# Kernel tuning notes

Measured on AMD Instinct MI355X. Metric: run time of the kernel, lower is better.

The kernel has to match this reference:

```python
import jax, jax.numpy as jnp
import numpy as np
import math

B, S, HID = 2, 2048, 512
H, HKV, QB, VB = 8, 2, 8, 16
W = 256 // QB            # suffix window size = 32
QKD = W * QB             # unfolded qk dim = 256
TAU = 1.0


def setup_inputs() -> dict:
    key = jax.random.key(0)
    ks = jax.random.split(key, 7)
    return {
        "hidden_states": jax.random.normal(ks[0], (B, S, HID), jnp.float32),
        "Wq": jax.random.normal(ks[1], (H * QB, HID), jnp.float32) * (HID ** -0.5),
        "Wk": jax.random.normal(ks[2], (HKV * QB, HID), jnp.float32) * (HID ** -0.5),
        "Wv": jax.random.normal(ks[3], (HKV * VB, HID), jnp.float32) * (HID ** -0.5),
        "Wo": jax.random.normal(ks[4], (HID, H * VB), jnp.float32) * ((H * VB) ** -0.5),
        "v_emb0": jnp.full((H * VB,), -1e-5, jnp.float32),
        "v_emb1": jnp.full((H * VB,), +1e-5, jnp.float32),
    }


def _forward(hidden_states, Wq, Wk, Wv, Wo, v_emb0, v_emb1):
    b, s, _ = hidden_states.shape
    # bit-quantized (soft) q/k/v projections
    q = jnp.tanh((hidden_states @ Wq.T) / TAU).reshape(b, s, H, QB).transpose(0, 2, 1, 3)      # [B,H,S,QB]
    k = jnp.tanh((hidden_states @ Wk.T) / TAU).reshape(b, s, HKV, QB).transpose(0, 2, 1, 3)    # [B,HKV,S,QB]
    v = jax.nn.sigmoid((hidden_states @ Wv.T) / TAU).reshape(b, s, HKV, VB).transpose(0, 2, 1, 3)
    # suffix shift of values: F.pad(v, (0,0,-1,1)) -> v[t] <- v[t+1], last position zero
    v = jnp.concatenate([v[:, :, 1:], jnp.zeros_like(v[:, :, :1])], axis=2)                    # [B,HKV,S,VB]
    # left-pad seq by W-1 zeros, then unfold sliding windows of length W
    pad = ((0, 0), (0, 0), (W - 1, 0), (0, 0))
    qp, kp = jnp.pad(q, pad), jnp.pad(k, pad)
    win = jnp.arange(s)[:, None] + jnp.arange(W)[None, :]   # [S,W] window indices into padded seq
    qw = qp[:, :, win, :].reshape(b, H, s, QKD)             # concat window positions x bits
    kw = kp[:, :, win, :].reshape(b, HKV, s, QKD)
    # GQA: repeat kv heads
    rep = H // HKV
    kw = jnp.repeat(kw, rep, axis=1)
    vr = jnp.repeat(v, rep, axis=1)
    scale = 1.0 / math.sqrt(QKD) / TAU
    # custom bias r_j / (r_i + 1) under strictly-causal mask (j < i)
    r = jnp.arange(s, dtype=hidden_states.dtype)
    mask = jnp.tril(jnp.ones((s, s), dtype=bool), -1)
    bias = jnp.where(mask, (r[None, :] / (r[:, None] + 1.0)) / TAU, 0.0)
    scores = jnp.einsum('bhqd,bhkd->bhqk', qw, kw) * scale + bias
    neg = jnp.finfo(scores.dtype).min
    scores = jnp.where(mask, scores, neg)
    # stable masked softmax (fully-masked row 0 -> zero weights instead of NaN)
    scores = scores - jax.lax.stop_gradient(jnp.max(scores, axis=-1, keepdims=True))
    e = jnp.exp(scores) * mask
    attn = e / jnp.maximum(jnp.sum(e, axis=-1, keepdims=True), 1e-30)
    out = jnp.einsum('bhqk,bhkd->bhqd', attn, vr)           # [B,H,S,VB]
    out = out.transpose(0, 2, 1, 3).reshape(b, s, H * VB)
    # learned emb0/emb1 interpolation
    out = out * v_emb1 + (1.0 - out) * v_emb0
    return out @ Wo.T


def reference(hidden_states, Wq, Wk, Wv, Wo, v_emb0, v_emb1):
    return _forward(hidden_states, Wq, Wk, Wv, Wo, v_emb0, v_emb1)
```

## Files before the change

### kernel.cpp

```cpp
#include <hip/hip_runtime.h>
#include <hip/hip_bf16.h>

typedef unsigned int u32;
typedef unsigned short u16;
typedef float f32x4 __attribute__((ext_vector_type(4)));
typedef short s16x8 __attribute__((ext_vector_type(8)));

#define B_   2
#define S_   2048
#define HID_ 512
#define H_   8
#define HKV_ 2
#define QB_  8
#define VB_  16
#define NQ_  64
#define HVB_ 128
#define LOG2E_ 1.4426950408889634f
#define MFIX2_ 24.525815695089866f

__device__ __forceinline__ u16 f2bf(float f) {
    u32 b = __builtin_bit_cast(u32, f);
    b += 0x7FFFu + ((b >> 16) & 1u);
    return (u16)(b >> 16);
}
__device__ __forceinline__ u16 bf16u(float f) {
    return __builtin_bit_cast(u16, (__bf16)f);
}
__device__ __forceinline__ f32x4 mfma16(s16x8 a, s16x8 b, f32x4 c) {
    return __builtin_amdgcn_mfma_f32_16x16x32_bf16(a, b, c, 0, 0, 0);
}
__device__ __forceinline__ float fast_tanh(float x) {
    float e = exp2f(x * (2.f * LOG2E_));
    return 1.f - 2.f * __builtin_amdgcn_rcpf(e + 1.f);
}
__device__ __forceinline__ float fast_sigmoid(float x) {
    return __builtin_amdgcn_rcpf(1.f + exp2f(-LOG2E_ * x));
}

__global__ void k0_convert(const float* __restrict__ Wq, const float* __restrict__ Wk,
                           const float* __restrict__ Wv, const float* __restrict__ Wo,
                           u16* __restrict__ Wc, u16* __restrict__ Wob) {
    int idx = blockIdx.x * 256 + threadIdx.x;
    {
        int n = idx >> 9, k = idx & 511;
        float v = (n < NQ_) ? Wq[n * HID_ + k]
                : (n < NQ_ + 16) ? Wk[(n - NQ_) * HID_ + k]
                : (n < 112) ? Wv[(n - NQ_ - 16) * HID_ + k] : 0.f;
        Wc[idx] = f2bf(v);
    }
    Wob[idx] = f2bf(Wo[idx]);
}

__global__ __launch_bounds__(256) void k1_proj(
    const float* __restrict__ hidden, const u16* __restrict__ Wc,
    u16* __restrict__ qb, u16* __restrict__ kb, u16* __restrict__ vt)
{
    const int tid = threadIdx.x;
    const int r0 = blockIdx.x * 16;
    const int wv = tid >> 6, lane = tid & 63;
    const int li = lane & 15, lo4 = lane >> 4;

    const float* hrow = hidden + (r0 + li) * HID_;

    f32x4 acc[2];
    acc[0] = (f32x4){0.f, 0.f, 0.f, 0.f};
    acc[1] = (f32x4){0.f, 0.f, 0.f, 0.f};

    #pragma unroll
    for (int kc = 0; kc < 16; ++kc) {
        f32x4 x0 = *(const f32x4*)&hrow[32 * kc + 8 * lo4];
        f32x4 x1 = *(const f32x4*)&hrow[32 * kc + 8 * lo4 + 4];
        s16x8 a = { (short)f2bf(x0[0]), (short)f2bf(x0[1]), (short)f2bf(x0[2]), (short)f2bf(x0[3]),
                    (short)f2bf(x1[0]), (short)f2bf(x1[1]), (short)f2bf(x1[2]), (short)f2bf(x1[3]) };
        #pragma unroll
        for (int u = 0; u < 2; ++u) {
            int n = (wv + 4 * u) * 16 + li;
            s16x8 bfr = *(const s16x8*)&Wc[n * HID_ + 32 * kc + 8 * lo4];
            acc[u] = mfma16(a, bfr, acc[u]);
        }
    }

    #pragma unroll
    for (int u = 0; u < 2; ++u) {
        int n = (wv + 4 * u) * 16 + li;
        if (n < 112) {
            #pragma unroll
            for (int reg = 0; reg < 4; ++reg) {
                int gs = r0 + 4 * lo4 + reg;
                int b = gs >> 11, s = gs & 2047;
                float pre = acc[u][reg];
                if (n < NQ_) {
                    int h = n >> 3, bit = n & 7;
                    qb[(((b * H_ + h) * S_) + s) * QB_ + bit] =
                        f2bf(fast_tanh(pre) * (0.0625f * LOG2E_));
                } else if (n < NQ_ + 16) {
                    int nk = n - NQ_;
                    kb[(((b * HKV_ + (nk >> 3)) * S_) + s) * QB_ + (nk & 7)] = f2bf(fast_tanh(pre));
                } else {
                    int nv = n - NQ_ - 16;
                    int hv = nv >> 4, vb = nv & 15;
                    u16 sig = f2bf(fast_sigmoid(pre));
                    if (s > 0)
                        vt[((b * HKV_ + hv) * VB_ + vb) * S_ + (s - 1)] = sig;
                    if (s == S_ - 1)
                        vt[((b * HKV_ + hv) * VB_ + vb) * S_ + (S_ - 1)] = 0;
                }
            }
        }
    }
}

__global__ __launch_bounds__(256, 2) void k2_attn(
    const u16* __restrict__ qb, const u16* __restrict__ kb, const u16* __restrict__ vt,
    const float* __restrict__ vemb0, const float* __restrict__ vemb1,
    u16* __restrict__ AO)
{
    __shared__ __align__(16) u16 psa[4][32 * 72];
    __shared__ float Om[4][2][16][16];
    __shared__ float lv[4][2][16];

    const int bid = blockIdx.x;
    const int rb = bid >> 4;
    const int r  = (rb < 32) ? (63 - rb) : (rb - 32);
    const int I0 = r * 32;
    const int nJ = ((I0 + 30) >> 6) + 1;
    const int bh = bid & 15;
    const int b = bh >> 3, h = bh & 7, hkv = h >> 2;

    const int g = threadIdx.x >> 6;
    const int lane = threadIdx.x & 63;
    const int li = lane & 15, lo4 = lane >> 4;

    u16* psw = psa[g];
    const u16* kpl = kb + ((b * HKV_ + hkv) * S_) * QB_ + (li + lo4 - 31) * QB_;
    const u16* vtp = vt + ((b * HKV_ + hkv) * VB_) * S_ + li * S_ + 8 * lo4;

    s16x8 qf[2][8];
    #pragma unroll
    for (int ig = 0; ig < 2; ++ig) {
        const int gr0 = I0 + 16 * ig + li - 31 + lo4;
        const u16* qp = qb + ((b * H_ + h) * S_) * QB_ + gr0 * QB_;
        #pragma unroll
        for (int kk = 0; kk < 8; ++kk) {
            s16x8 v = {0, 0, 0, 0, 0, 0, 0, 0};
            if (gr0 + 4 * kk >= 0) v = *(const s16x8*)(qp + kk * 32);
            qf[ig][kk] = v;
        }
    }

    int ibase[2];
    float binv[2][4];
    #pragma unroll
    for (int ig = 0; ig < 2; ++ig) {
        ibase[ig] = I0 + 16 * ig + 4 * lo4;
        #pragma unroll
        for (int reg = 0; reg < 4; ++reg) {
            float d = (float)(ibase[ig] + reg + 1);
            float rc = __builtin_amdgcn_rcpf(d);
            rc = rc * (2.f - d * rc);
            binv[ig][reg] = rc * LOG2E_;
        }
    }

    f32x4 O[2];
    O[0] = (f32x4){0.f, 0.f, 0.f, 0.f};
    O[1] = (f32x4){0.f, 0.f, 0.f, 0.f};
    float lsum[2][4] = {{0.f, 0.f, 0.f, 0.f}, {0.f, 0.f, 0.f, 0.f}};

    s16x8 ld[20];
    {
        const u16* kt = kpl + g * 512;
        if (g == 0) {
            #pragma unroll
            for (int m = 0; m < 20; ++m) {
                s16x8 v = {0, 0, 0, 0, 0, 0, 0, 0};
                if (li + lo4 + 4 * m >= 31) v = *(const s16x8*)(kt + 32 * m);
                ld[m] = v;
            }
        } else {
            #pragma unroll
            for (int m = 0; m < 20; ++m)
                ld[m] = *(const s16x8*)(kt + 32 * m);
        }
    }

    for (int jt = g; jt < nJ; jt += 4) {
        const int J0 = jt * 64;

        s16x8 vfr0 = *(const s16x8*)(vtp + J0);
        s16x8 vfr1 = *(const s16x8*)(vtp + J0 + 32);

        f32x4 sacc[2][4];
        #pragma unroll
        for (int ig = 0; ig < 2; ++ig)
            #pragma unroll
            for (int ns = 0; ns < 4; ++ns)
                sacc[ig][ns] = (f32x4){0.f, 0.f, 0.f, 0.f};
        #pragma unroll
        for (int m = 0; m < 20; ++m) {
            s16x8 f = ld[m];
            {
                int kk = m & 3, ns = m >> 2;
                if (ns < 4) {
                    sacc[0][ns] = mfma16(qf[0][kk], f, sacc[0][ns]);
                    sacc[1][ns] = mfma16(qf[1][kk], f, sacc[1][ns]);
                }
            }
            {
                int kk = (m & 3) + 4, ns = (m >> 2) - 1;
                if (ns >= 0) {
                    sacc[0][ns] = mfma16(qf[0][kk], f, sacc[0][ns]);
                    sacc[1][ns] = mfma16(qf[1][kk], f, sacc[1][ns]);
                }
            }
        }

        if (jt + 4 < nJ) {
            const u16* kt = kpl + (jt + 4) * 512;
            #pragma unroll
            for (int m = 0; m < 20; ++m)
                ld[m] = *(const s16x8*)(kt + 32 * m);
        }

        const float jlif = (float)(J0 + li);
        #pragma unroll
        for (int ig = 0; ig < 2; ++ig) {
            const bool edgev = (J0 + 63) >= (I0 + 16 * ig);
            #pragma unroll
            for (int reg = 0; reg < 4; ++reg) {
                const int irow = ibase[ig] + reg;
                const float bi = binv[ig][reg];
                float p[4];
                #pragma unroll
                for (int ns = 0; ns < 4; ++ns) {
                    float bns = fmaf(jlif + (float)(16 * ns), bi, -MFIX2_);
                    float e = exp2f(sacc[ig][ns][reg] + bns);
                    if (edgev)
                        e = (J0 + 16 * ns + li < irow) ? e : 0.f;
                    p[ns] = e;
                }
                lsum[ig][reg] += (p[0] + p[1]) + (p[2] + p[3]);
                #pragma unroll
                for (int ns = 0; ns < 4; ++ns)
                    psw[(ig * 16 + 4 * lo4 + reg) * 72 + 16 * ns + li] = bf16u(p[ns]);
            }
        }

        #pragma unroll
        for (int ig = 0; ig < 2; ++ig) {
            s16x8 pa0 = *(const s16x8*)&psw[(ig * 16 + li) * 72 + 8 * lo4];
            s16x8 pa1 = *(const s16x8*)&psw[(ig * 16 + li) * 72 + 32 + 8 * lo4];
            O[ig] = mfma16(pa0, vfr0, O[ig]);
            O[ig] = mfma16(pa1, vfr1, O[ig]);
        }
    }

    #pragma unroll
    for (int ig = 0; ig < 2; ++ig) {
        #pragma unroll
        for (int reg = 0; reg < 4; ++reg) {
            float l = lsum[ig][reg];
            l += __shfl_xor(l, 1);
            l += __shfl_xor(l, 2);
            l += __shfl_xor(l, 4);
            l += __shfl_xor(l, 8);
            Om[g][ig][4 * lo4 + reg][li] = O[ig][reg];
            if (li == 0) lv[g][ig][4 * lo4 + reg] = l;
        }
    }
    __syncthreads();

    if (g == 0) {
        const int hc = h * VB_ + li;
        const float e0 = vemb0[hc], e1 = vemb1[hc];
        #pragma unroll
        for (int ig = 0; ig < 2; ++ig) {
            #pragma unroll
            for (int reg = 0; reg < 4; ++reg) {
                const int row = 4 * lo4 + reg;
                float Oc = (Om[0][ig][row][li] + Om[1][ig][row][li])
                         + (Om[2][ig][row][li] + Om[3][ig][row][li]);
                float lc = (lv[0][ig][row] + lv[1][ig][row])
                         + (lv[2][ig][row] + lv[3][ig][row]);
                float lr = fmaxf(lc, 1e-30f);
                float rinv = __builtin_amdgcn_rcpf(lr);
                rinv = rinv * (2.f - lr * rinv);
                float o = Oc * rinv;
                const int s = I0 + 16 * ig + row;
                AO[(b * S_ + s) * HVB_ + hc] = f2bf(e0 + o * (e1 - e0));
            }
        }
    }
}

__global__ __launch_bounds__(256) void k3_out(
    const u16* __restrict__ AO, const u16* __restrict__ Wob,
    float* __restrict__ out)
{
    const int tid = threadIdx.x;
    const int r0 = (blockIdx.x >> 2) * 16;
    const int cg = blockIdx.x & 3;
    const int wv = tid >> 6, lane = tid & 63;
    const int li = lane & 15, lo4 = lane >> 4;

    const u16* arow = AO + (r0 + li) * HVB_;

    f32x4 acc[2];
    acc[0] = (f32x4){0.f, 0.f, 0.f, 0.f};
    acc[1] = (f32x4){0.f, 0.f, 0.f, 0.f};

    #pragma unroll
    for (int kc = 0; kc < 4; ++kc) {
        s16x8 a = *(const s16x8*)&arow[32 * kc + 8 * lo4];
        #pragma unroll
        for (int u = 0; u < 2; ++u) {
            int o = cg * 128 + (wv + 4 * u) * 16 + li;
            s16x8 bfr = *(const s16x8*)&Wob[o * HVB_ + 32 * kc + 8 * lo4];
            acc[u] = mfma16(a, bfr, acc[u]);
        }
    }

    #pragma unroll
    for (int u = 0; u < 2; ++u) {
        int o = cg * 128 + (wv + 4 * u) * 16 + li;
        #pragma unroll
        for (int reg = 0; reg < 4; ++reg)
            out[(r0 + 4 * lo4 + reg) * HID_ + o] = acc[u][reg];
    }
}

extern "C" void kernel_launch(void* const* d_in, const int* in_sizes, int n_in,
                              void* d_out, int out_size, void* d_ws, size_t ws_size,
                              hipStream_t stream)
{
    (void)in_sizes; (void)n_in; (void)out_size;
    const float* hidden = (const float*)d_in[0];
    const float* Wq = (const float*)d_in[1];
    const float* Wk = (const float*)d_in[2];
    const float* Wv = (const float*)d_in[3];
    const float* Wo = (const float*)d_in[4];
    const float* ve0 = (const float*)d_in[5];
    const float* ve1 = (const float*)d_in[6];
    float* out = (float*)d_out;

    char* base = (char*)d_ws;
    u16* qb  = (u16*)(base);
    u16* kb  = (u16*)(base + 524288);
    u16* vt  = (u16*)(base + 655360);
    u16* AO  = (u16*)(base + 917504);
    u16* Wc  = (u16*)(base + 1966080);
    u16* Wob = (u16*)(base + 2097152);
    if (ws_size < 2228224) return;

    hipLaunchKernelGGL(k0_convert, dim3(256), dim3(256), 0, stream,
                       Wq, Wk, Wv, Wo, Wc, Wob);
    hipLaunchKernelGGL(k1_proj, dim3(256), dim3(256), 0, stream,
                       hidden, Wc, qb, kb, vt);
    hipLaunchKernelGGL(k2_attn, dim3(1024), dim3(256), 0, stream,
                       qb, kb, vt, ve0, ve1, AO);
    hipLaunchKernelGGL(k3_out, dim3(1024), dim3(256), 0, stream,
                       AO, Wob, out);
}
```

Baseline: 62.90 us.

## Split attention KV range across blocks with partial-sum merge kernel

```diff
diff --git a/kernel.cpp b/kernel.cpp
--- a/kernel.cpp
+++ b/kernel.cpp
@@ -17,12 +17,8 @@
 #define HVB_ 128
 #define LOG2E_ 1.4426950408889634f
 #define MFIX2_ 24.525815695089866f
-
-__device__ __forceinline__ u16 f2bf(float f) {
-    u32 b = __builtin_bit_cast(u32, f);
-    b += 0x7FFFu + ((b >> 16) & 1u);
-    return (u16)(b >> 16);
-}
+#define PSLOT_ 544
+
 __device__ __forceinline__ u16 bf16u(float f) {
     return __builtin_bit_cast(u16, (__bf16)f);
 }
@@ -46,9 +42,9 @@
         float v = (n < NQ_) ? Wq[n * HID_ + k]
                 : (n < NQ_ + 16) ? Wk[(n - NQ_) * HID_ + k]
                 : (n < 112) ? Wv[(n - NQ_ - 16) * HID_ + k] : 0.f;
-        Wc[idx] = f2bf(v);
-    }
-    Wob[idx] = f2bf(Wo[idx]);
+        Wc[idx] = bf16u(v);
+    }
+    Wob[idx] = bf16u(Wo[idx]);
 }
 
 __global__ __launch_bounds__(256) void k1_proj(
@@ -56,75 +52,69 @@
     u16* __restrict__ qb, u16* __restrict__ kb, u16* __restrict__ vt)
 {
     const int tid = threadIdx.x;
-    const int r0 = blockIdx.x * 16;
+    const int r0 = (int)(blockIdx.x >> 1) * 16;
     const int wv = tid >> 6, lane = tid & 63;
     const int li = lane & 15, lo4 = lane >> 4;
+    const int fr = (blockIdx.x & 1) * 4 + wv;
+    if (fr >= 7) return;
+    const int n = fr * 16 + li;
 
     const float* hrow = hidden + (r0 + li) * HID_;
-
-    f32x4 acc[2];
-    acc[0] = (f32x4){0.f, 0.f, 0.f, 0.f};
-    acc[1] = (f32x4){0.f, 0.f, 0.f, 0.f};
+    f32x4 acc = (f32x4){0.f, 0.f, 0.f, 0.f};
 
     #pragma unroll
     for (int kc = 0; kc < 16; ++kc) {
         f32x4 x0 = *(const f32x4*)&hrow[32 * kc + 8 * lo4];
         f32x4 x1 = *(const f32x4*)&hrow[32 * kc + 8 * lo4 + 4];
-        s16x8 a = { (short)f2bf(x0[0]), (short)f2bf(x0[1]), (short)f2bf(x0[2]), (short)f2bf(x0[3]),
-                    (short)f2bf(x1[0]), (short)f2bf(x1[1]), (short)f2bf(x1[2]), (short)f2bf(x1[3]) };
-        #pragma unroll
-        for (int u = 0; u < 2; ++u) {
-            int n = (wv + 4 * u) * 16 + li;
-            s16x8 bfr = *(const s16x8*)&Wc[n * HID_ + 32 * kc + 8 * lo4];
-            acc[u] = mfma16(a, bfr, acc[u]);
-        }
-    }
-
-    #pragma unroll
-    for (int u = 0; u < 2; ++u) {
-        int n = (wv + 4 * u) * 16 + li;
-        if (n < 112) {
-            #pragma unroll
-            for (int reg = 0; reg < 4; ++reg) {
-                int gs = r0 + 4 * lo4 + reg;
-                int b = gs >> 11, s = gs & 2047;
-                float pre = acc[u][reg];
-                if (n < NQ_) {
-                    int h = n >> 3, bit = n & 7;
-                    qb[(((b * H_ + h) * S_) + s) * QB_ + bit] =
-                        f2bf(fast_tanh(pre) * (0.0625f * LOG2E_));
-                } else if (n < NQ_ + 16) {
-                    int nk = n - NQ_;
-                    kb[(((b * HKV_ + (nk >> 3)) * S_) + s) * QB_ + (nk & 7)] = f2bf(fast_tanh(pre));
-                } else {
-                    int nv = n - NQ_ - 16;
-                    int hv = nv >> 4, vb = nv & 15;
-                    u16 sig = f2bf(fast_sigmoid(pre));
-                    if (s > 0)
-                        vt[((b * HKV_ + hv) * VB_ + vb) * S_ + (s - 1)] = sig;
-                    if (s == S_ - 1)
-                        vt[((b * HKV_ + hv) * VB_ + vb) * S_ + (S_ - 1)] = 0;
-                }
-            }
+        s16x8 a = { (short)bf16u(x0[0]), (short)bf16u(x0[1]), (short)bf16u(x0[2]), (short)bf16u(x0[3]),
+                    (short)bf16u(x1[0]), (short)bf16u(x1[1]), (short)bf16u(x1[2]), (short)bf16u(x1[3]) };
+        s16x8 bfr = *(const s16x8*)&Wc[n * HID_ + 32 * kc + 8 * lo4];
+        acc = mfma16(a, bfr, acc);
+    }
+
+    #pragma unroll
+    for (int reg = 0; reg < 4; ++reg) {
+        int gs = r0 + 4 * lo4 + reg;
+        int b = gs >> 11, s = gs & 2047;
+        float pre = acc[reg];
+        if (n < NQ_) {
+            int h = n >> 3, bit = n & 7;
+            qb[(((b * H_ + h) * S_) + s) * QB_ + bit] =
+                bf16u(fast_tanh(pre) * (0.0625f * LOG2E_));
+        } else if (n < NQ_ + 16) {
+            int nk = n - NQ_;
+            kb[(((b * HKV_ + (nk >> 3)) * S_) + s) * QB_ + (nk & 7)] = bf16u(fast_tanh(pre));
+        } else {
+            int nv = n - NQ_ - 16;
+            int hv = nv >> 4, vb = nv & 15;
+            u16 sig = bf16u(fast_sigmoid(pre));
+            if (s > 0)
+                vt[((b * HKV_ + hv) * VB_ + vb) * S_ + (s - 1)] = sig;
+            if (s == S_ - 1)
+                vt[((b * HKV_ + hv) * VB_ + vb) * S_ + (S_ - 1)] = 0;
         }
     }
 }
 
 __global__ __launch_bounds__(256, 2) void k2_attn(
     const u16* __restrict__ qb, const u16* __restrict__ kb, const u16* __restrict__ vt,
-    const float* __restrict__ vemb0, const float* __restrict__ vemb1,
-    u16* __restrict__ AO)
+    float* __restrict__ part)
 {
     __shared__ __align__(16) u16 psa[4][32 * 72];
     __shared__ float Om[4][2][16][16];
     __shared__ float lv[4][2][16];
 
     const int bid = blockIdx.x;
-    const int rb = bid >> 4;
-    const int r  = (rb < 32) ? (63 - rb) : (rb - 32);
+    const int bh = bid & 15;
+    const int wk = bid >> 4;
+    int r, c;
+    if (wk < 16)      { r = wk;                    c = 0; }
+    else if (wk < 48) { r = 16 + ((wk - 16) >> 1); c = (wk - 16) & 1; }
+    else if (wk < 96) { r = 32 + (wk - 48) / 3;    c = (wk - 48) % 3; }
+    else              { r = 48 + ((wk - 96) >> 2); c = (wk - 96) & 3; }
+
     const int I0 = r * 32;
-    const int nJ = ((I0 + 30) >> 6) + 1;
-    const int bh = bid & 15;
+    const int nJ = (r >> 1) + 1;
     const int b = bh >> 3, h = bh & 7, hkv = h >> 2;
 
     const int g = threadIdx.x >> 6;
@@ -135,16 +125,15 @@
     const u16* kpl = kb + ((b * HKV_ + hkv) * S_) * QB_ + (li + lo4 - 31) * QB_;
     const u16* vtp = vt + ((b * HKV_ + hkv) * VB_) * S_ + li * S_ + 8 * lo4;
 
-    s16x8 qf[2][8];
-    #pragma unroll
-    for (int ig = 0; ig < 2; ++ig) {
-        const int gr0 = I0 + 16 * ig + li - 31 + lo4;
+    s16x8 qfu[12];
+    {
+        const int gr0 = I0 + li - 31 + lo4;
         const u16* qp = qb + ((b * H_ + h) * S_) * QB_ + gr0 * QB_;
         #pragma unroll
-        for (int kk = 0; kk < 8; ++kk) {
+        for (int m = 0; m < 12; ++m) {
             s16x8 v = {0, 0, 0, 0, 0, 0, 0, 0};
-            if (gr0 + 4 * kk >= 0) v = *(const s16x8*)(qp + kk * 32);
-            qf[ig][kk] = v;
+            if (gr0 + 4 * m >= 0) v = *(const s16x8*)(qp + m * 32);
+            qfu[m] = v;
         }
     }
 
@@ -167,91 +156,98 @@
     O[1] = (f32x4){0.f, 0.f, 0.f, 0.f};
     float lsum[2][4] = {{0.f, 0.f, 0.f, 0.f}, {0.f, 0.f, 0.f, 0.f}};
 
-    s16x8 ld[20];
-    {
-        const u16* kt = kpl + g * 512;
-        if (g == 0) {
+    #pragma unroll
+    for (int t = 0; t < 2; ++t) {
+        const int jt = 8 * c + g + 4 * t;
+        if (jt < nJ) {
+            const int J0 = jt * 64;
+
+            s16x8 vfr0 = *(const s16x8*)(vtp + J0);
+            s16x8 vfr1 = *(const s16x8*)(vtp + J0 + 32);
+
+            f32x4 sacc[2][4];
             #pragma unroll
-            for (int m = 0; m < 20; ++m) {
-                s16x8 v = {0, 0, 0, 0, 0, 0, 0, 0};
-                if (li + lo4 + 4 * m >= 31) v = *(const s16x8*)(kt + 32 * m);
-                ld[m] = v;
-            }
-        } else {
-            #pragma unroll
-            for (int m = 0; m < 20; ++m)
-                ld[m] = *(const s16x8*)(kt + 32 * m);
-        }
-    }
-
-    for (int jt = g; jt < nJ; jt += 4) {
-        const int J0 = jt * 64;
-
-        s16x8 vfr0 = *(const s16x8*)(vtp + J0);
-        s16x8 vfr1 = *(const s16x8*)(vtp + J0 + 32);
-
-        f32x4 sacc[2][4];
-        #pragma unroll
-        for (int ig = 0; ig < 2; ++ig)
-            #pragma unroll
-            for (int ns = 0; ns < 4; ++ns)
-                sacc[ig][ns] = (f32x4){0.f, 0.f, 0.f, 0.f};
-        #pragma unroll
-        for (int m = 0; m < 20; ++m) {
-            s16x8 f = ld[m];
-            {
-                int kk = m & 3, ns = m >> 2;
-                if (ns < 4) {
-                    sacc[0][ns] = mfma16(qf[0][kk], f, sacc[0][ns]);
-                    sacc[1][ns] = mfma16(qf[1][kk], f, sacc[1][ns]);
+            for (int ig = 0; ig < 2; ++ig)
+                #pragma unroll
+                for (int ns = 0; ns < 4; ++ns)
+                    sacc[ig][ns] = (f32x4){0.f, 0.f, 0.f, 0.f};
+
+            const u16* kt = kpl + jt * 512;
+            if (jt == 0) {
+                #pragma unroll
+                for (int c5 = 0; c5 < 5; ++c5) {
+                    s16x8 f[4];
+                    #pragma unroll
+                    for (int j = 0; j < 4; ++j) {
+                        int m = 4 * c5 + j;
+                        s16x8 v = {0, 0, 0, 0, 0, 0, 0, 0};
+                        if (li + lo4 + 4 * m >= 31) v = *(const s16x8*)(kt + 32 * m);
+                        f[j] = v;
+                    }
+                    #pragma unroll
+                    for (int j = 0; j < 4; ++j) {
+                        if (c5 < 4) {
+                            sacc[0][c5] = mfma16(qfu[j],     f[j], sacc[0][c5]);
+                            sacc[1][c5] = mfma16(qfu[j + 4], f[j], sacc[1][c5]);
+                        }
+                        if (c5 >= 1) {
+                            sacc[0][c5 - 1] = mfma16(qfu[j + 4], f[j], sacc[0][c5 - 1]);
+                            sacc[1][c5 - 1] = mfma16(qfu[j + 8], f[j], sacc[1][c5 - 1]);
+                        }
+                    }
+                }
+            } else {
+                #pragma unroll
+                for (int c5 = 0; c5 < 5; ++c5) {
+                    s16x8 f[4];
+                    #pragma unroll
+                    for (int j = 0; j < 4; ++j)
+                        f[j] = *(const s16x8*)(kt + 32 * (4 * c5 + j));
+                    #pragma unroll
+                    for (int j = 0; j < 4; ++j) {
+                        if (c5 < 4) {
+                            sacc[0][c5] = mfma16(qfu[j],     f[j], sacc[0][c5]);
+                            sacc[1][c5] = mfma16(qfu[j + 4], f[j], sacc[1][c5]);
+                        }
+                        if (c5 >= 1) {
+                            sacc[0][c5 - 1] = mfma16(qfu[j + 4], f[j], sacc[0][c5 - 1]);
+                            sacc[1][c5 - 1] = mfma16(qfu[j + 8], f[j], sacc[1][c5 - 1]);
+                        }
+                    }
                 }
             }
-            {
-                int kk = (m & 3) + 4, ns = (m >> 2) - 1;
-                if (ns >= 0) {
-                    sacc[0][ns] = mfma16(qf[0][kk], f, sacc[0][ns]);
-                    sacc[1][ns] = mfma16(qf[1][kk], f, sacc[1][ns]);
+
+            const float jlif = (float)(J0 + li);
+            #pragma unroll
+            for (int ig = 0; ig < 2; ++ig) {
+                const bool edgev = (J0 + 63) >= (I0 + 16 * ig);
+                #pragma unroll
+                for (int reg = 0; reg < 4; ++reg) {
+                    const int irow = ibase[ig] + reg;
+                    const float bi = binv[ig][reg];
+                    float p[4];
+                    #pragma unroll
+                    for (int ns = 0; ns < 4; ++ns) {
+                        float bns = fmaf(jlif + (float)(16 * ns), bi, -MFIX2_);
+                        float e = exp2f(sacc[ig][ns][reg] + bns);
+                        if (edgev)
+                            e = (J0 + 16 * ns + li < irow) ? e : 0.f;
+                        p[ns] = e;
+                    }
+                    lsum[ig][reg] += (p[0] + p[1]) + (p[2] + p[3]);
+                    #pragma unroll
+                    for (int ns = 0; ns < 4; ++ns)
+                        psw[(ig * 16 + 4 * lo4 + reg) * 72 + 16 * ns + li] = bf16u(p[ns]);
                 }
             }
-        }
-
-        if (jt + 4 < nJ) {
-            const u16* kt = kpl + (jt + 4) * 512;
+
             #pragma unroll
-            for (int m = 0; m < 20; ++m)
-                ld[m] = *(const s16x8*)(kt + 32 * m);
-        }
-
-        const float jlif = (float)(J0 + li);
-        #pragma unroll
-        for (int ig = 0; ig < 2; ++ig) {
-            const bool edgev = (J0 + 63) >= (I0 + 16 * ig);
-            #pragma unroll
-            for (int reg = 0; reg < 4; ++reg) {
-                const int irow = ibase[ig] + reg;
-                const float bi = binv[ig][reg];
-                float p[4];
-                #pragma unroll
-                for (int ns = 0; ns < 4; ++ns) {
-                    float bns = fmaf(jlif + (float)(16 * ns), bi, -MFIX2_);
-                    float e = exp2f(sacc[ig][ns][reg] + bns);
-                    if (edgev)
-                        e = (J0 + 16 * ns + li < irow) ? e : 0.f;
-                    p[ns] = e;
-                }
-                lsum[ig][reg] += (p[0] + p[1]) + (p[2] + p[3]);
-                #pragma unroll
-                for (int ns = 0; ns < 4; ++ns)
-                    psw[(ig * 16 + 4 * lo4 + reg) * 72 + 16 * ns + li] = bf16u(p[ns]);
+            for (int ig = 0; ig < 2; ++ig) {
+                s16x8 pa0 = *(const s16x8*)&psw[(ig * 16 + li) * 72 + 8 * lo4];
+                s16x8 pa1 = *(const s16x8*)&psw[(ig * 16 + li) * 72 + 32 + 8 * lo4];
+                O[ig] = mfma16(pa0, vfr0, O[ig]);
+                O[ig] = mfma16(pa1, vfr1, O[ig]);
             }
-        }
-
-        #pragma unroll
-        for (int ig = 0; ig < 2; ++ig) {
-            s16x8 pa0 = *(const s16x8*)&psw[(ig * 16 + li) * 72 + 8 * lo4];
-            s16x8 pa1 = *(const s16x8*)&psw[(ig * 16 + li) * 72 + 32 + 8 * lo4];
-            O[ig] = mfma16(pa0, vfr0, O[ig]);
-            O[ig] = mfma16(pa1, vfr1, O[ig]);
         }
     }
 
@@ -271,26 +267,52 @@
     __syncthreads();
 
     if (g == 0) {
-        const int hc = h * VB_ + li;
-        const float e0 = vemb0[hc], e1 = vemb1[hc];
+        float* ps = part + (size_t)((bh * 64 + r) * 4 + c) * PSLOT_;
         #pragma unroll
         for (int ig = 0; ig < 2; ++ig) {
             #pragma unroll
             for (int reg = 0; reg < 4; ++reg) {
-                const int row = 4 * lo4 + reg;
-                float Oc = (Om[0][ig][row][li] + Om[1][ig][row][li])
-                         + (Om[2][ig][row][li] + Om[3][ig][row][li]);
-                float lc = (lv[0][ig][row] + lv[1][ig][row])
-                         + (lv[2][ig][row] + lv[3][ig][row]);
-                float lr = fmaxf(lc, 1e-30f);
-                float rinv = __builtin_amdgcn_rcpf(lr);
-                rinv = rinv * (2.f - lr * rinv);
-                float o = Oc * rinv;
-                const int s = I0 + 16 * ig + row;
-                AO[(b * S_ + s) * HVB_ + hc] = f2bf(e0 + o * (e1 - e0));
+                const int rw16 = 4 * lo4 + reg;
+                const int row = 16 * ig + rw16;
+                float Oc = (Om[0][ig][rw16][li] + Om[1][ig][rw16][li])
+                         + (Om[2][ig][rw16][li] + Om[3][ig][rw16][li]);
+                ps[row * 16 + li] = Oc;
+                if (li == 0) {
+                    float lc = (lv[0][ig][rw16] + lv[1][ig][rw16])
+                             + (lv[2][ig][rw16] + lv[3][ig][rw16]);
+                    ps[512 + row] = lc;
+                }
             }
         }
     }
+}
+
+__global__ __launch_bounds__(512) void k2b_merge(
+    const float* __restrict__ part,
+    const float* __restrict__ vemb0, const float* __restrict__ vemb1,
+    u16* __restrict__ AO)
+{
+    const int bid = blockIdx.x;
+    const int r = bid >> 4, bh = bid & 15;
+    const int b = bh >> 3, h = bh & 7;
+    const int nc = (r < 16) ? 1 : ((r >> 4) + 1);
+    const int t = threadIdx.x;
+    const int row = t >> 4, col = t & 15;
+
+    const float* ps = part + (size_t)((bh * 64 + r) * 4) * PSLOT_;
+    float Osum = 0.f, lsum = 0.f;
+    for (int c = 0; c < nc; ++c) {
+        Osum += ps[c * PSLOT_ + row * 16 + col];
+        lsum += ps[c * PSLOT_ + 512 + row];
+    }
+    const int hc = h * VB_ + col;
+    float e0 = vemb0[hc], e1 = vemb1[hc];
+    float lr = fmaxf(lsum, 1e-30f);
+    float rinv = __builtin_amdgcn_rcpf(lr);
+    rinv = rinv * (2.f - lr * rinv);
+    float o = Osum * rinv;
+    const int s = r * 32 + row;
+    AO[(b * S_ + s) * HVB_ + hc] = bf16u(e0 + o * (e1 - e0));
 }
 
 __global__ __launch_bounds__(256) void k3_out(
@@ -298,35 +320,25 @@
     float* __restrict__ out)
 {
     const int tid = threadIdx.x;
-    const int r0 = (blockIdx.x >> 2) * 16;
-    const int cg = blockIdx.x & 3;
+    const int r0 = (int)(blockIdx.x >> 3) * 16;
+    const int cg = blockIdx.x & 7;
     const int wv = tid >> 6, lane = tid & 63;
     const int li = lane & 15, lo4 = lane >> 4;
+    const int o = cg * 64 + wv * 16 + li;
 
     const u16* arow = AO + (r0 + li) * HVB_;
-
-    f32x4 acc[2];
-    acc[0] = (f32x4){0.f, 0.f, 0.f, 0.f};
-    acc[1] = (f32x4){0.f, 0.f, 0.f, 0.f};
+    f32x4 acc = (f32x4){0.f, 0.f, 0.f, 0.f};
 
     #pragma unroll
     for (int kc = 0; kc < 4; ++kc) {
         s16x8 a = *(const s16x8*)&arow[32 * kc + 8 * lo4];
-        #pragma unroll
-        for (int u = 0; u < 2; ++u) {
-            int o = cg * 128 + (wv + 4 * u) * 16 + li;
-            s16x8 bfr = *(const s16x8*)&Wob[o * HVB_ + 32 * kc + 8 * lo4];
-            acc[u] = mfma16(a, bfr, acc[u]);
-        }
-    }
-
-    #pragma unroll
-    for (int u = 0; u < 2; ++u) {
-        int o = cg * 128 + (wv + 4 * u) * 16 + li;
-        #pragma unroll
-        for (int reg = 0; reg < 4; ++reg)
-            out[(r0 + 4 * lo4 + reg) * HID_ + o] = acc[u][reg];
-    }
+        s16x8 bfr = *(const s16x8*)&Wob[o * HVB_ + 32 * kc + 8 * lo4];
+        acc = mfma16(a, bfr, acc);
+    }
+
+    #pragma unroll
+    for (int reg = 0; reg < 4; ++reg)
+        out[(r0 + 4 * lo4 + reg) * HID_ + o] = acc[reg];
 }
 
 extern "C" void kernel_launch(void* const* d_in, const int* in_sizes, int n_in,
@@ -344,20 +356,23 @@
     float* out = (float*)d_out;
 
     char* base = (char*)d_ws;
-    u16* qb  = (u16*)(base);
-    u16* kb  = (u16*)(base + 524288);
-    u16* vt  = (u16*)(base + 655360);
-    u16* AO  = (u16*)(base + 917504);
-    u16* Wc  = (u16*)(base + 1966080);
-    u16* Wob = (u16*)(base + 2097152);
-    if (ws_size < 2228224) return;
+    u16* qb   = (u16*)(base);
+    u16* kb   = (u16*)(base + 524288);
+    u16* vt   = (u16*)(base + 655360);
+    u16* AO   = (u16*)(base + 917504);
+    u16* Wc   = (u16*)(base + 1966080);
+    u16* Wob  = (u16*)(base + 2097152);
+    float* part = (float*)(base + 2228224);
+    if (ws_size < 11141120u) return;
 
     hipLaunchKernelGGL(k0_convert, dim3(256), dim3(256), 0, stream,
                        Wq, Wk, Wv, Wo, Wc, Wob);
-    hipLaunchKernelGGL(k1_proj, dim3(256), dim3(256), 0, stream,
+    hipLaunchKernelGGL(k1_proj, dim3(512), dim3(256), 0, stream,
                        hidden, Wc, qb, kb, vt);
-    hipLaunchKernelGGL(k2_attn, dim3(1024), dim3(256), 0, stream,
-                       qb, kb, vt, ve0, ve1, AO);
-    hipLaunchKernelGGL(k3_out, dim3(1024), dim3(256), 0, stream,
+    hipLaunchKernelGGL(k2_attn, dim3(2560), dim3(256), 0, stream,
+                       qb, kb, vt, part);
+    hipLaunchKernelGGL(k2b_merge, dim3(1024), dim3(512), 0, stream,
+                       part, ve0, ve1, AO);
+    hipLaunchKernelGGL(k3_out, dim3(2048), dim3(256), 0, stream,
                        AO, Wob, out);
 }
```

New measurement: 78.18 us. 24.3% more time.
